# Optimization experiments

Hardware: AMD Instinct MI355X
Metric: run time of the kernel (lower is better)

## Reference

```python
import jax, jax.numpy as jnp
import numpy as np

DIM = 1024
HEADS = 16
HEAD_DIM = DIM // HEADS
MLP_HIDDEN = 4 * DIM
OUT_DIM = 1000
V_DIM = 1024
EPS = 1e-5
SCALE = DIM ** -0.5  # note: module scales by hidden_dim**-0.5, not head_dim**-0.5


def layer_norm(x, g, b):
    mu = jnp.mean(x, axis=-1, keepdims=True)
    var = jnp.mean(jnp.square(x - mu), axis=-1, keepdims=True)
    return (x - mu) * jax.lax.rsqrt(var + EPS) * g + b


def setup_inputs() -> dict:
    key = jax.random.key(0)
    ks = jax.random.split(key, 12)
    B, N = 4, 2048
    s = lambda fan_in: 1.0 / np.sqrt(fan_in)
    return {
        "x": jax.random.normal(ks[0], (B, N, DIM), jnp.float32),
        "value": jax.random.normal(ks[1], (B, N, V_DIM), jnp.float32),
        "wq": jax.random.normal(ks[2], (DIM, DIM), jnp.float32) * s(DIM),
        "wk": jax.random.normal(ks[3], (DIM, DIM), jnp.float32) * s(DIM),
        "wv": jax.random.normal(ks[4], (V_DIM, DIM), jnp.float32) * s(V_DIM),
        "w_ap": jax.random.normal(ks[5], (DIM, DIM), jnp.float32) * s(DIM),
        "b_ap": jnp.zeros((DIM,), jnp.float32),
        "g1": jnp.ones((DIM,), jnp.float32),
        "be1": jnp.zeros((DIM,), jnp.float32),
        "g2": jnp.ones((DIM,), jnp.float32),
        "be2": jnp.zeros((DIM,), jnp.float32),
        "w1": jax.random.normal(ks[6], (DIM, MLP_HIDDEN), jnp.float32) * s(DIM),
        "b1": jnp.zeros((MLP_HIDDEN,), jnp.float32),
        "w2": jax.random.normal(ks[7], (MLP_HIDDEN, DIM), jnp.float32) * s(MLP_HIDDEN),
        "b2": jnp.zeros((DIM,), jnp.float32),
        "w_out": jax.random.normal(ks[8], (DIM, OUT_DIM), jnp.float32) * s(DIM),
        "b_out": jnp.zeros((OUT_DIM,), jnp.float32),
    }


def reference(x, value, wq, wk, wv, w_ap, b_ap, g1, be1, g2, be2, w1, b1, w2, b2, w_out, b_out):
    B, N, C = x.shape
    xn = layer_norm(x, g1, be1)                      # [B,N,C]
    q = (xn @ wq).reshape(B, N, HEADS, HEAD_DIM)     # query and key both from norm1(x)
    k = (xn @ wk).reshape(B, N, HEADS, HEAD_DIM)
    v = (value @ wv).reshape(B, N, HEADS, HEAD_DIM)
    attn = jnp.einsum("bqhd,bkhd->bhqk", q, k) * SCALE
    attn = jax.nn.softmax(attn, axis=-1)
    o = jnp.einsum("bhqk,bkhd->bqhd", attn, v).reshape(B, N, C)
    x = x + (o @ w_ap + b_ap)                        # residual (dropouts are identity)
    h = jax.nn.gelu(layer_norm(x, g2, be2) @ w1 + b1, approximate=False)
    x = x + (h @ w2 + b2)
    return jax.nn.softmax(x @ w_out + b_out, axis=2)
```

## Files before the change

### kernel.cpp

```cpp
#include <hip/hip_runtime.h>
#include <math.h>

typedef unsigned short u16;
typedef unsigned int u32;
typedef __attribute__((ext_vector_type(4))) float f32x4;
typedef __attribute__((ext_vector_type(4))) int i32x4;
typedef __attribute__((ext_vector_type(8))) short short8;
typedef __attribute__((ext_vector_type(4))) unsigned short u16x4;
typedef __attribute__((ext_vector_type(4))) __fp16 f16x4;
typedef __attribute__((ext_vector_type(2))) __fp16 f16x2;

#define DEV __device__ __forceinline__

DEV u16 f2bf(float f) {
  unsigned u = __float_as_uint(f);
  u += 0x7FFFu + ((u >> 16) & 1u);
  return (u16)(u >> 16);
}

DEV float fexp2(float x) {
  float r;
  asm("v_exp_f32 %0, %1" : "=v"(r) : "v"(x));
  return r;
}

DEV void gload_lds16(const void* g, void* l) {
  __builtin_amdgcn_global_load_lds((const __attribute__((address_space(1))) void*)g,
                                   (__attribute__((address_space(3))) void*)l, 16, 0, 0);
}

template<int N> DEV void waitv() {
  if constexpr (N == 8)      asm volatile("s_waitcnt vmcnt(8)" ::: "memory");
  else if constexpr (N == 6) asm volatile("s_waitcnt vmcnt(6)" ::: "memory");
  else if constexpr (N == 4) asm volatile("s_waitcnt vmcnt(4)" ::: "memory");
  else if constexpr (N == 3) asm volatile("s_waitcnt vmcnt(3)" ::: "memory");
  else                       asm volatile("s_waitcnt vmcnt(0)" ::: "memory");
}

DEV void block_fence() {
  __builtin_amdgcn_s_barrier();
  __builtin_amdgcn_sched_barrier(0);
  asm volatile("" ::: "memory");
}

enum { EPI_QK = 0, EPI_VT = 1, EPI_RESID_F32 = 2, EPI_GELU = 3, EPI_RESID_BF16 = 4, EPI_LOGITS = 5 };

__global__ void transpose_w(const float* __restrict__ in, u16* __restrict__ out,
                            int K, int Nsrc, int Nout) {
  __shared__ float tile[32][33];
  int k0 = blockIdx.x * 32, n0 = blockIdx.y * 32;
  int tx = threadIdx.x, ty = threadIdx.y;
#pragma unroll
  for (int i = 0; i < 4; ++i) {
    int k = k0 + ty + i * 8, n = n0 + tx;
    tile[ty + i * 8][tx] = (n < Nsrc) ? in[(size_t)k * Nsrc + n] : 0.0f;
  }
  __syncthreads();
#pragma unroll
  for (int i = 0; i < 4; ++i) {
    int n = n0 + ty + i * 8, k = k0 + tx;
    out[(size_t)n * K + k] = f2bf(tile[tx][ty + i * 8]);
  }
}

__global__ void convert_bf16(const float* __restrict__ in, u16* __restrict__ out, int n4) {
  int i = blockIdx.x * blockDim.x + threadIdx.x;
  int stride = gridDim.x * blockDim.x;
  for (int j = i; j < n4; j += stride) {
    f32x4 v = reinterpret_cast<const f32x4*>(in)[j];
    u16x4 o;
    o[0] = f2bf(v[0]); o[1] = f2bf(v[1]); o[2] = f2bf(v[2]); o[3] = f2bf(v[3]);
    reinterpret_cast<u16x4*>(out)[j] = o;
  }
}

DEV float blockReduceSum(float v) {
  __shared__ float red[4];
#pragma unroll
  for (int m = 32; m >= 1; m >>= 1) v += __shfl_xor(v, m);
  __syncthreads();
  if ((threadIdx.x & 63) == 0) red[threadIdx.x >> 6] = v;
  __syncthreads();
  return red[0] + red[1] + red[2] + red[3];
}

DEV float blockReduceMax(float v) {
  __shared__ float redm[4];
#pragma unroll
  for (int m = 32; m >= 1; m >>= 1) v = fmaxf(v, __shfl_xor(v, m));
  __syncthreads();
  if ((threadIdx.x & 63) == 0) redm[threadIdx.x >> 6] = v;
  __syncthreads();
  return fmaxf(fmaxf(redm[0], redm[1]), fmaxf(redm[2], redm[3]));
}

__global__ __launch_bounds__(256)
void layernorm_k(const float* __restrict__ x, const float* __restrict__ g,
                 const float* __restrict__ b, u16* __restrict__ out) {
  int row = blockIdx.x, t = threadIdx.x;
  const float* xr = x + (size_t)row * 1024;
  f32x4 v = *reinterpret_cast<const f32x4*>(xr + t * 4);
  float mu = blockReduceSum(v[0] + v[1] + v[2] + v[3]) * (1.0f / 1024.0f);
  f32x4 d;
  d[0] = v[0] - mu; d[1] = v[1] - mu; d[2] = v[2] - mu; d[3] = v[3] - mu;
  float var = blockReduceSum(d[0]*d[0] + d[1]*d[1] + d[2]*d[2] + d[3]*d[3]) * (1.0f / 1024.0f);
  float rstd = rsqrtf(var + 1e-5f);
  u16x4 o;
#pragma unroll
  for (int i = 0; i < 4; ++i) o[i] = f2bf(d[i] * rstd * g[t * 4 + i] + b[t * 4 + i]);
  *reinterpret_cast<u16x4*>(out + (size_t)row * 1024 + t * 4) = o;
}

__global__ __launch_bounds__(256)
void softmax_rows(float* __restrict__ io) {
  int row = blockIdx.x, t = threadIdx.x;
  float* p = io + (size_t)row * 1000;
  float v[4];
  float mx = -INFINITY;
#pragma unroll
  for (int i = 0; i < 4; ++i) {
    int c = t + i * 256;
    v[i] = (c < 1000) ? p[c] : -INFINITY;
    mx = fmaxf(mx, v[i]);
  }
  mx = blockReduceMax(mx);
  float s = 0.f;
#pragma unroll
  for (int i = 0; i < 4; ++i) {
    int c = t + i * 256;
    v[i] = (c < 1000) ? __expf(v[i] - mx) : 0.f;
    s += v[i];
  }
  s = blockReduceSum(s);
  float inv = 1.0f / s;
#pragma unroll
  for (int i = 0; i < 4; ++i) {
    int c = t + i * 256;
    if (c < 1000) p[c] = v[i] * inv;
  }
}

template<int EPI, int BN>
__global__ __launch_bounds__(512, 1)
void gemm_pipe(const u16* __restrict__ A, const u16* __restrict__ Bt,
               void* __restrict__ outp, const float* __restrict__ aux0,
               const float* __restrict__ aux1, int M, int N, int K, float scale) {
  constexpr int ASZ = 256 * 32;
  constexpr int BSZ = BN * 32;
  constexpr int NJ  = BN / 64;
  constexpr int LPT = (BN == 256) ? 4 : 3;
  __shared__ u16 lds[4][ASZ + BSZ];

  const int t = threadIdx.x;
  const int lane = t & 63;
  const int w = t >> 6;
  const int wm = w >> 2, wn = w & 3;
  const int bm = blockIdx.y * 256, bn = blockIdx.x * BN;
  const int l15 = lane & 15, lg = lane >> 4;
  const int nk = K >> 5;

  f32x4 acc[8][NJ] = {};

  auto STAGE = [&](int buf, int kt) {
    const int k0 = kt * 32;
#pragma unroll
    for (int p = 0; p < 2; ++p) {
      int c = p * 512 + t;
      int r = c >> 2, s0 = c & 3;
      int ss = s0 ^ ((r >> 1) & 3);
      gload_lds16(A + (size_t)(bm + r) * K + k0 + ss * 8, &lds[buf][c * 8]);
    }
    if constexpr (BN == 256) {
#pragma unroll
      for (int p = 0; p < 2; ++p) {
        int c = p * 512 + t;
        int r = c >> 2, s0 = c & 3;
        int ss = s0 ^ ((r >> 1) & 3);
        gload_lds16(Bt + (size_t)(bn + r) * K + k0 + ss * 8, &lds[buf][ASZ + c * 8]);
      }
    } else {
      int r = t >> 2, s0 = t & 3;
      int ss = s0 ^ ((r >> 1) & 3);
      gload_lds16(Bt + (size_t)(bn + r) * K + k0 + ss * 8, &lds[buf][ASZ + t * 8]);
    }
  };

  STAGE(0, 0);
  STAGE(1, 1);
  STAGE(2, 2);
  waitv<2 * LPT>();
  block_fence();

#pragma unroll 1
  for (int tt = 0; tt < nk; ++tt) {
    const int buf = tt & 3;
    short8 af[8], bf[NJ];
#pragma unroll
    for (int i = 0; i < 8; ++i) {
      int rA = wm * 128 + i * 16 + l15;
      af[i] = *reinterpret_cast<const short8*>(&lds[buf][rA * 32 + (lg ^ ((rA >> 1) & 3)) * 8]);
    }
#pragma unroll
    for (int j = 0; j < NJ; ++j) {
      int rB = wn * (BN / 4) + j * 16 + l15;
      bf[j] = *reinterpret_cast<const short8*>(&lds[buf][ASZ + rB * 32 + (lg ^ ((rB >> 1) & 3)) * 8]);
    }
    if (tt + 3 < nk) STAGE((tt + 3) & 3, tt + 3);

    __builtin_amdgcn_s_setprio(1);
#pragma unroll
    for (int i = 0; i < 8; ++i)
#pragma unroll
      for (int j = 0; j < NJ; ++j)
        acc[i][j] = __builtin_amdgcn_mfma_f32_16x16x32_bf16(af[i], bf[j], acc[i][j], 0, 0, 0);
    __builtin_amdgcn_s_setprio(0);

    if (tt + 3 < nk)      waitv<2 * LPT>();
    else if (tt + 2 < nk) waitv<LPT>();
    else if (tt + 1 < nk) waitv<0>();
    block_fence();
  }

#pragma unroll
  for (int i = 0; i < 8; ++i)
#pragma unroll
    for (int j = 0; j < NJ; ++j)
#pragma unroll
      for (int r = 0; r < 4; ++r) {
        int row = bm + wm * 128 + i * 16 + lg * 4 + r;
        int col = bn + wn * (BN / 4) + j * 16 + l15;
        float v = acc[i][j][r];
        if constexpr (EPI == EPI_QK) {
          float sc = (col < 1024) ? 0.03125f : 1.0f;
          ((u16*)outp)[(size_t)row * 2048 + col] = f2bf(v * sc);
        } else if constexpr (EPI == EPI_VT) {
          size_t idx = ((size_t)((row >> 11) * 16 + (col >> 6)) * 64 + (col & 63)) * 2048 + (row & 2047);
          __fp16 hv = (__fp16)v;
          ((u16*)outp)[idx] = *reinterpret_cast<u16*>(&hv);
        } else if constexpr (EPI == EPI_RESID_F32) {
          ((float*)outp)[(size_t)row * N + col] = v + aux0[col] + aux1[(size_t)row * N + col];
        } else if constexpr (EPI == EPI_GELU) {
          float tt2 = v + aux0[col];
          float u = tt2 * (0.7978845608f + 0.035677408f * tt2 * tt2);
          float e = fexp2(u * 2.8853900818f);
          float gl = tt2 * (1.0f - 1.0f / (1.0f + e));
          ((u16*)outp)[(size_t)row * N + col] = f2bf(gl);
        } else if constexpr (EPI == EPI_RESID_BF16) {
          float tt2 = v + aux0[col] + aux1[(size_t)row * N + col];
          ((u16*)outp)[(size_t)row * N + col] = f2bf(tt2);
        } else {
          if (col < 1000) ((float*)outp)[(size_t)row * 1000 + col] = v + aux0[col];
        }
      }
  (void)scale; (void)aux0; (void)aux1; (void)M;
}

__global__ __launch_bounds__(512)
void attn_flash(const u16* __restrict__ QKb, const u16* __restrict__ Vt,
                u16* __restrict__ Ob) {
  __shared__ u16 Ks[2][128 * 64];
  __shared__ u16 Vs[2][64 * 128];
  const int t = threadIdx.x;
  const int lane = t & 63, w = t >> 6;
  const int l15 = lane & 15, lg = lane >> 4;
  const int bh = blockIdx.x;
  const int b = bh >> 4, h = bh & 15;
  const int qrow0 = b * 2048 + blockIdx.y * 128 + w * 16;

  short8 qf[2];
#pragma unroll
  for (int ks = 0; ks < 2; ++ks)
    qf[ks] = *reinterpret_cast<const short8*>(QKb + (size_t)(qrow0 + l15) * 2048 + h * 64 + ks * 32 + lg * 8);

  f32x4 oacc[4] = {};
  float lpart = 0.f;

  const int sgK = ((t & 7) ^ ((t >> 3) & 7)) * 8;
  const int sgV = ((t & 15) ^ ((t >> 4) & 7)) * 8;
  const int tk8 = t * 8;

  auto STAGE = [&](int buf, int tt) {
    int kt = tt * 128;
#pragma unroll
    for (int p = 0; p < 2; ++p) {
      int rK = p * 64 + (t >> 3);
      gload_lds16(QKb + (size_t)(b * 2048 + kt + rK) * 2048 + 1024 + h * 64 + sgK, &Ks[buf][p * 4096 + tk8]);
      int rV = p * 32 + (t >> 4);
      gload_lds16(Vt + ((size_t)bh * 64 + rV) * 2048 + kt + sgV, &Vs[buf][p * 4096 + tk8]);
    }
  };

  auto COMPUTE = [&](int buf) {
    f32x4 s[8];
#pragma unroll
    for (int cb = 0; cb < 8; ++cb) {
      s[cb] = f32x4{0.f, 0.f, 0.f, 0.f};
      int rK = cb * 16 + l15;
#pragma unroll
      for (int ks = 0; ks < 2; ++ks) {
        int sk = (lg + ks * 4) ^ (rK & 7);
        short8 kf = *reinterpret_cast<const short8*>(&Ks[buf][rK * 64 + sk * 8]);
        s[cb] = __builtin_amdgcn_mfma_f32_16x16x32_bf16(kf, qf[ks], s[cb], 0, 0, 0);
      }
    }

    const float L2E = 1.44269504088896f;
    const char* vbase = (const char*)&Vs[buf][0];
#pragma unroll
    for (int cb = 0; cb < 8; ++cb) {
      float e0 = fexp2(s[cb][0] * L2E), e1 = fexp2(s[cb][1] * L2E);
      float e2 = fexp2(s[cb][2] * L2E), e3 = fexp2(s[cb][3] * L2E);
      lpart += (e0 + e1) + (e2 + e3);
      f16x2 plo = __builtin_amdgcn_cvt_pkrtz(e0, e1);
      f16x2 phi = __builtin_amdgcn_cvt_pkrtz(e2, e3);
      f16x4 pf;
      pf[0] = plo[0]; pf[1] = plo[1]; pf[2] = phi[0]; pf[3] = phi[1];
#pragma unroll
      for (int db = 0; db < 4; ++db) {
        int d = db * 16 + l15;
        int boff = d * 256 + ((((2 * cb + (lg >> 1)) ^ (d & 7)) << 4) | ((lg & 1) << 3));
        f16x4 vf = *reinterpret_cast<const f16x4*>(vbase + boff);
        oacc[db] = __builtin_amdgcn_mfma_f32_16x16x16f16(pf, vf, oacc[db], 0, 0, 0);
      }
    }
  };

  STAGE(0, 0);
  __syncthreads();
#pragma unroll 1
  for (int i = 0; i < 8; ++i) {
    STAGE(1, 2 * i + 1);
    COMPUTE(0);
    __syncthreads();
    if (i < 7) STAGE(0, 2 * i + 2);
    COMPUTE(1);
    __syncthreads();
  }

  lpart += __shfl_xor(lpart, 16);
  lpart += __shfl_xor(lpart, 32);
  float inv = 1.0f / lpart;
  float invr[4];
#pragma unroll
  for (int r = 0; r < 4; ++r) invr[r] = __shfl(inv, lg * 4 + r);

#pragma unroll
  for (int db = 0; db < 4; ++db)
#pragma unroll
    for (int r = 0; r < 4; ++r) {
      int row = qrow0 + lg * 4 + r;
      int col = h * 64 + db * 16 + l15;
      Ob[(size_t)row * 1024 + col] = f2bf(oacc[db][r] * invr[r]);
    }
}

extern "C" void kernel_launch(void* const* d_in, const int* in_sizes, int n_in,
                              void* d_out, int out_size, void* d_ws, size_t ws_size,
                              hipStream_t stream) {
  (void)in_sizes; (void)n_in; (void)out_size; (void)ws_size;
  const float* x     = (const float*)d_in[0];
  const float* value = (const float*)d_in[1];
  const float* wq    = (const float*)d_in[2];
  const float* wk    = (const float*)d_in[3];
  const float* wv    = (const float*)d_in[4];
  const float* w_ap  = (const float*)d_in[5];
  const float* b_ap  = (const float*)d_in[6];
  const float* g1    = (const float*)d_in[7];
  const float* be1   = (const float*)d_in[8];
  const float* g2    = (const float*)d_in[9];
  const float* be2   = (const float*)d_in[10];
  const float* w1    = (const float*)d_in[11];
  const float* b1    = (const float*)d_in[12];
  const float* w2    = (const float*)d_in[13];
  const float* b2    = (const float*)d_in[14];
  const float* w_out = (const float*)d_in[15];
  const float* b_out = (const float*)d_in[16];

  char* ws = (char*)d_ws;
  u16* wqT   = (u16*)(ws + 0x0000000);
  u16* wkT   = (u16*)(ws + 0x0200000);
  u16* wvT   = (u16*)(ws + 0x0400000);
  u16* wapT  = (u16*)(ws + 0x0600000);
  u16* woutT = (u16*)(ws + 0x0800000);
  u16* w1T   = (u16*)(ws + 0x0A00000);
  u16* w2T   = (u16*)(ws + 0x1200000);
  u16* xn    = (u16*)(ws + 0x1A00000);
  u16* valb  = (u16*)(ws + 0x2A00000);
  u16* qkb   = (u16*)(ws + 0x3A00000);
  u16* vT    = (u16*)(ws + 0x5A00000);
  u16* ob    = (u16*)(ws + 0x6A00000);
  float* x1  = (float*)(ws + 0x7A00000);
  u16* hb    = valb;
  u16* xn2   = xn;
  u16* x2b   = ob;

  dim3 tb(32, 8);
  transpose_w<<<dim3(32, 32),  tb, 0, stream>>>(wq,    wqT,   1024, 1024, 1024);
  transpose_w<<<dim3(32, 32),  tb, 0, stream>>>(wk,    wkT,   1024, 1024, 1024);
  transpose_w<<<dim3(32, 32),  tb, 0, stream>>>(wv,    wvT,   1024, 1024, 1024);
  transpose_w<<<dim3(32, 32),  tb, 0, stream>>>(w_ap,  wapT,  1024, 1024, 1024);
  transpose_w<<<dim3(32, 32),  tb, 0, stream>>>(w_out, woutT, 1024, 1000, 1024);
  transpose_w<<<dim3(32, 128), tb, 0, stream>>>(w1,    w1T,   1024, 4096, 4096);
  transpose_w<<<dim3(128, 32), tb, 0, stream>>>(w2,    w2T,   4096, 1024, 1024);

  convert_bf16<<<2048, 256, 0, stream>>>(value, valb, 2097152);
  layernorm_k<<<8192, 256, 0, stream>>>(x, g1, be1, xn);

  gemm_pipe<EPI_QK, 256><<<dim3(8, 32),  512, 0, stream>>>(xn,   wqT, qkb, nullptr, nullptr, 8192, 2048, 1024, 1.0f);
  gemm_pipe<EPI_VT, 128><<<dim3(8, 32),  512, 0, stream>>>(valb, wvT, vT,  nullptr, nullptr, 8192, 1024, 1024, 1.0f);

  attn_flash<<<dim3(64, 16), 512, 0, stream>>>(qkb, vT, ob);

  gemm_pipe<EPI_RESID_F32, 128><<<dim3(8, 32),  512, 0, stream>>>(ob,  wapT, x1, b_ap, x, 8192, 1024, 1024, 1.0f);
  layernorm_k<<<8192, 256, 0, stream>>>(x1, g2, be2, xn2);
  gemm_pipe<EPI_GELU, 256>     <<<dim3(16, 32), 512, 0, stream>>>(xn2, w1T, hb, b1, nullptr, 8192, 4096, 1024, 1.0f);
  gemm_pipe<EPI_RESID_BF16, 128><<<dim3(8, 32), 512, 0, stream>>>(hb,  w2T, x2b, b2, x1, 8192, 1024, 4096, 1.0f);
  gemm_pipe<EPI_LOGITS, 128>   <<<dim3(8, 32),  512, 0, stream>>>(x2b, woutT, (float*)d_out, b_out, nullptr, 8192, 1024, 1024, 1.0f);
  softmax_rows<<<8192, 256, 0, stream>>>((float*)d_out);
}
```

Measured before the change: 468.1 us.

## Rewrite GEMM as double-buffered K=64 phased pipeline; fold log2e into Q scale

Replaces the 4-stage K=32 GEMM pipeline with a double-buffered K=64 tile scheme. Each iteration is split into phases that interleave sub-tile LDS reads, prefetch loads for the next tile and MFMA batches, separated by barriers. The aim is to hide global load latency behind compute while halving the number of K iterations, at the cost of more barriers and a shallower prefetch depth. It also folds the log2(e) factor into the Q scaling so the attention kernel skips one multiply per exponent.

```diff
diff --git a/kernel.cpp b/kernel.cpp
--- a/kernel.cpp
+++ b/kernel.cpp
@@ -30,10 +30,9 @@
 }
 
 template<int N> DEV void waitv() {
-  if constexpr (N == 8)      asm volatile("s_waitcnt vmcnt(8)" ::: "memory");
-  else if constexpr (N == 6) asm volatile("s_waitcnt vmcnt(6)" ::: "memory");
-  else if constexpr (N == 4) asm volatile("s_waitcnt vmcnt(4)" ::: "memory");
+  if constexpr (N == 4)      asm volatile("s_waitcnt vmcnt(4)" ::: "memory");
   else if constexpr (N == 3) asm volatile("s_waitcnt vmcnt(3)" ::: "memory");
+  else if constexpr (N == 2) asm volatile("s_waitcnt vmcnt(2)" ::: "memory");
   else                       asm volatile("s_waitcnt vmcnt(0)" ::: "memory");
 }
 
@@ -142,14 +141,12 @@
 
 template<int EPI, int BN>
 __global__ __launch_bounds__(512, 1)
-void gemm_pipe(const u16* __restrict__ A, const u16* __restrict__ Bt,
-               void* __restrict__ outp, const float* __restrict__ aux0,
-               const float* __restrict__ aux1, int M, int N, int K, float scale) {
-  constexpr int ASZ = 256 * 32;
-  constexpr int BSZ = BN * 32;
-  constexpr int NJ  = BN / 64;
-  constexpr int LPT = (BN == 256) ? 4 : 3;
-  __shared__ u16 lds[4][ASZ + BSZ];
+void gemm_8ph(const u16* __restrict__ A, const u16* __restrict__ Bt,
+              void* __restrict__ outp, const float* __restrict__ aux0,
+              const float* __restrict__ aux1, int M, int N, int K, float scale) {
+  constexpr int NJ = BN / 64;
+  __shared__ u16 As[2][256 * 64];
+  __shared__ u16 Bs[2][BN * 64];
 
   const int t = threadIdx.x;
   const int lane = t & 63;
@@ -157,68 +154,98 @@
   const int wm = w >> 2, wn = w & 3;
   const int bm = blockIdx.y * 256, bn = blockIdx.x * BN;
   const int l15 = lane & 15, lg = lane >> 4;
-  const int nk = K >> 5;
+  const int nt = K >> 6;
 
   f32x4 acc[8][NJ] = {};
-
-  auto STAGE = [&](int buf, int kt) {
-    const int k0 = kt * 32;
-#pragma unroll
-    for (int p = 0; p < 2; ++p) {
-      int c = p * 512 + t;
-      int r = c >> 2, s0 = c & 3;
-      int ss = s0 ^ ((r >> 1) & 3);
-      gload_lds16(A + (size_t)(bm + r) * K + k0 + ss * 8, &lds[buf][c * 8]);
-    }
+  short8 aR[4][2], bR[2][2];
+
+  auto stA = [&](int buf, int kt, int q) {
+    int rl = q * 64 + (t >> 3), s0 = t & 7;
+    gload_lds16(A + (size_t)(bm + rl) * K + kt * 64 + (s0 ^ (rl & 7)) * 8,
+                &As[buf][q * 4096 + t * 8]);
+  };
+  auto stB = [&](int buf, int kt, int q) {
+    int rl = q * 64 + (t >> 3), s0 = t & 7;
+    gload_lds16(Bt + (size_t)(bn + rl) * K + kt * 64 + (s0 ^ (rl & 7)) * 8,
+                &Bs[buf][q * 4096 + t * 8]);
+  };
+  auto rdA = [&](int buf, int mh) {
+#pragma unroll
+    for (int i2 = 0; i2 < 4; ++i2) {
+      int rA = wm * 128 + mh * 64 + i2 * 16 + l15;
+#pragma unroll
+      for (int ks = 0; ks < 2; ++ks)
+        aR[i2][ks] = *reinterpret_cast<const short8*>(
+            &As[buf][rA * 64 + (((ks * 4 + lg) ^ (rA & 7)) * 8)]);
+    }
+  };
+  auto rdB = [&](int buf, int nh) {
+#pragma unroll
+    for (int j2 = 0; j2 < 2; ++j2) {
+      int rB = (BN == 256) ? (wn * 64 + nh * 32 + j2 * 16 + l15)
+                           : (wn * 32 + j2 * 16 + l15);
+#pragma unroll
+      for (int ks = 0; ks < 2; ++ks)
+        bR[j2][ks] = *reinterpret_cast<const short8*>(
+            &Bs[buf][rB * 64 + (((ks * 4 + lg) ^ (rB & 7)) * 8)]);
+    }
+  };
+  auto domfma = [&](int mh, int nh) {
+    __builtin_amdgcn_s_setprio(1);
+#pragma unroll
+    for (int i2 = 0; i2 < 4; ++i2)
+#pragma unroll
+      for (int j2 = 0; j2 < 2; ++j2)
+#pragma unroll
+        for (int ks = 0; ks < 2; ++ks)
+          acc[mh * 4 + i2][nh * 2 + j2] = __builtin_amdgcn_mfma_f32_16x16x32_bf16(
+              aR[i2][ks], bR[j2][ks], acc[mh * 4 + i2][nh * 2 + j2], 0, 0, 0);
+    __builtin_amdgcn_s_setprio(0);
+  };
+
+  if constexpr (BN == 256) {
+    stB(0, 0, 0); stB(0, 0, 1); stB(0, 0, 2); stB(0, 0, 3);
+    stA(0, 0, 0); stA(0, 0, 2); stA(0, 0, 1); stA(0, 0, 3);
+  } else {
+    stB(0, 0, 0); stB(0, 0, 1);
+    stA(0, 0, 0); stA(0, 0, 2); stA(0, 0, 1); stA(0, 0, 3);
+  }
+
+#pragma unroll 1
+  for (int tt = 0; tt < nt; ++tt) {
+    const int buf = tt & 1, nb = buf ^ 1;
+    const bool pf = (tt + 1 < nt);
     if constexpr (BN == 256) {
-#pragma unroll
-      for (int p = 0; p < 2; ++p) {
-        int c = p * 512 + t;
-        int r = c >> 2, s0 = c & 3;
-        int ss = s0 ^ ((r >> 1) & 3);
-        gload_lds16(Bt + (size_t)(bn + r) * K + k0 + ss * 8, &lds[buf][ASZ + c * 8]);
-      }
+      waitv<2>();
+      block_fence();
+      rdA(buf, 0); rdB(buf, 0);
+      if (pf) { stB(nb, tt + 1, 0); stB(nb, tt + 1, 1); }
+      domfma(0, 0);
+      block_fence();
+      rdB(buf, 1);
+      if (pf) { stB(nb, tt + 1, 2); stB(nb, tt + 1, 3); }
+      domfma(0, 1);
+      if (pf) waitv<4>(); else waitv<0>();
+      block_fence();
+      rdA(buf, 1);
+      if (pf) { stA(nb, tt + 1, 0); stA(nb, tt + 1, 2); }
+      domfma(1, 1);
+      block_fence();
+      rdB(buf, 0);
+      if (pf) { stA(nb, tt + 1, 1); stA(nb, tt + 1, 3); }
+      domfma(1, 0);
     } else {
-      int r = t >> 2, s0 = t & 3;
-      int ss = s0 ^ ((r >> 1) & 3);
-      gload_lds16(Bt + (size_t)(bn + r) * K + k0 + ss * 8, &lds[buf][ASZ + t * 8]);
-    }
-  };
-
-  STAGE(0, 0);
-  STAGE(1, 1);
-  STAGE(2, 2);
-  waitv<2 * LPT>();
-  block_fence();
-
-#pragma unroll 1
-  for (int tt = 0; tt < nk; ++tt) {
-    const int buf = tt & 3;
-    short8 af[8], bf[NJ];
-#pragma unroll
-    for (int i = 0; i < 8; ++i) {
-      int rA = wm * 128 + i * 16 + l15;
-      af[i] = *reinterpret_cast<const short8*>(&lds[buf][rA * 32 + (lg ^ ((rA >> 1) & 3)) * 8]);
-    }
-#pragma unroll
-    for (int j = 0; j < NJ; ++j) {
-      int rB = wn * (BN / 4) + j * 16 + l15;
-      bf[j] = *reinterpret_cast<const short8*>(&lds[buf][ASZ + rB * 32 + (lg ^ ((rB >> 1) & 3)) * 8]);
-    }
-    if (tt + 3 < nk) STAGE((tt + 3) & 3, tt + 3);
-
-    __builtin_amdgcn_s_setprio(1);
-#pragma unroll
-    for (int i = 0; i < 8; ++i)
-#pragma unroll
-      for (int j = 0; j < NJ; ++j)
-        acc[i][j] = __builtin_amdgcn_mfma_f32_16x16x32_bf16(af[i], bf[j], acc[i][j], 0, 0, 0);
-    __builtin_amdgcn_s_setprio(0);
-
-    if (tt + 3 < nk)      waitv<2 * LPT>();
-    else if (tt + 2 < nk) waitv<LPT>();
-    else if (tt + 1 < nk) waitv<0>();
-    block_fence();
+      waitv<2>();
+      block_fence();
+      rdA(buf, 0); rdB(buf, 0);
+      if (pf) { stB(nb, tt + 1, 0); stB(nb, tt + 1, 1); stA(nb, tt + 1, 0); }
+      domfma(0, 0);
+      if (pf) waitv<3>(); else waitv<0>();
+      block_fence();
+      rdA(buf, 1);
+      if (pf) { stA(nb, tt + 1, 2); stA(nb, tt + 1, 1); stA(nb, tt + 1, 3); }
+      domfma(1, 0);
+    }
   }
 
 #pragma unroll
@@ -231,7 +258,7 @@
         int col = bn + wn * (BN / 4) + j * 16 + l15;
         float v = acc[i][j][r];
         if constexpr (EPI == EPI_QK) {
-          float sc = (col < 1024) ? 0.03125f : 1.0f;
+          float sc = (col < 1024) ? 0.03125f * 1.44269504088896f : 1.0f;
           ((u16*)outp)[(size_t)row * 2048 + col] = f2bf(v * sc);
         } else if constexpr (EPI == EPI_VT) {
           size_t idx = ((size_t)((row >> 11) * 16 + (col >> 6)) * 64 + (col & 63)) * 2048 + (row & 2047);
@@ -304,12 +331,11 @@
       }
     }
 
-    const float L2E = 1.44269504088896f;
     const char* vbase = (const char*)&Vs[buf][0];
 #pragma unroll
     for (int cb = 0; cb < 8; ++cb) {
-      float e0 = fexp2(s[cb][0] * L2E), e1 = fexp2(s[cb][1] * L2E);
-      float e2 = fexp2(s[cb][2] * L2E), e3 = fexp2(s[cb][3] * L2E);
+      float e0 = fexp2(s[cb][0]), e1 = fexp2(s[cb][1]);
+      float e2 = fexp2(s[cb][2]), e3 = fexp2(s[cb][3]);
       lpart += (e0 + e1) + (e2 + e3);
       f16x2 plo = __builtin_amdgcn_cvt_pkrtz(e0, e1);
       f16x2 phi = __builtin_amdgcn_cvt_pkrtz(e2, e3);
@@ -406,15 +432,15 @@
   convert_bf16<<<2048, 256, 0, stream>>>(value, valb, 2097152);
   layernorm_k<<<8192, 256, 0, stream>>>(x, g1, be1, xn);
 
-  gemm_pipe<EPI_QK, 256><<<dim3(8, 32),  512, 0, stream>>>(xn,   wqT, qkb, nullptr, nullptr, 8192, 2048, 1024, 1.0f);
-  gemm_pipe<EPI_VT, 128><<<dim3(8, 32),  512, 0, stream>>>(valb, wvT, vT,  nullptr, nullptr, 8192, 1024, 1024, 1.0f);
+  gemm_8ph<EPI_QK, 256><<<dim3(8, 32),  512, 0, stream>>>(xn,   wqT, qkb, nullptr, nullptr, 8192, 2048, 1024, 1.0f);
+  gemm_8ph<EPI_VT, 128><<<dim3(8, 32),  512, 0, stream>>>(valb, wvT, vT,  nullptr, nullptr, 8192, 1024, 1024, 1.0f);
 
   attn_flash<<<dim3(64, 16), 512, 0, stream>>>(qkb, vT, ob);
 
-  gemm_pipe<EPI_RESID_F32, 128><<<dim3(8, 32),  512, 0, stream>>>(ob,  wapT, x1, b_ap, x, 8192, 1024, 1024, 1.0f);
+  gemm_8ph<EPI_RESID_F32, 128><<<dim3(8, 32),  512, 0, stream>>>(ob,  wapT, x1, b_ap, x, 8192, 1024, 1024, 1.0f);
   layernorm_k<<<8192, 256, 0, stream>>>(x1, g2, be2, xn2);
-  gemm_pipe<EPI_GELU, 256>     <<<dim3(16, 32), 512, 0, stream>>>(xn2, w1T, hb, b1, nullptr, 8192, 4096, 1024, 1.0f);
-  gemm_pipe<EPI_RESID_BF16, 128><<<dim3(8, 32), 512, 0, stream>>>(hb,  w2T, x2b, b2, x1, 8192, 1024, 4096, 1.0f);
-  gemm_pipe<EPI_LOGITS, 128>   <<<dim3(8, 32),  512, 0, stream>>>(x2b, woutT, (float*)d_out, b_out, nullptr, 8192, 1024, 1024, 1.0f);
+  gemm_8ph<EPI_GELU, 256>     <<<dim3(16, 32), 512, 0, stream>>>(xn2, w1T, hb, b1, nullptr, 8192, 4096, 1024, 1.0f);
+  gemm_8ph<EPI_RESID_BF16, 128><<<dim3(8, 32), 512, 0, stream>>>(hb,  w2T, x2b, b2, x1, 8192, 1024, 4096, 1.0f);
+  gemm_8ph<EPI_LOGITS, 128>   <<<dim3(8, 32),  512, 0, stream>>>(x2b, woutT, (float*)d_out, b_out, nullptr, 8192, 1024, 1024, 1.0f);
   softmax_rows<<<8192, 256, 0, stream>>>((float*)d_out);
 }
```

After: 453.5 us. 3.1% less time.
